# Optimization experiments

Hardware: AMD Instinct MI355X
Metric: run time of the kernel (lower is better)

The kernel has to match this reference:

```python
import jax, jax.numpy as jnp
import numpy as np

B, L, D, H = 16, 1024, 768, 12
PHD = D // H  # per-head dim = 64


def setup_inputs() -> dict:
    key = jax.random.key(0)
    ks = jax.random.split(key, 6)
    s = 0.02  # small init scale (xavier-like magnitude)
    return {
        "embeddings": jax.random.normal(ks[0], (B, L, D), jnp.float32),
        "pre_w": jax.random.normal(ks[1], (D, D), jnp.float32) * s,
        "pre_b": jnp.zeros((D,), jnp.float32),
        "psfs": jax.random.normal(ks[2], (H, 2 * L - 1, PHD), jnp.float32) * s,
        "post_w": jax.random.normal(ks[3], (D, D), jnp.float32) * s,
        "post_b": jnp.zeros((D,), jnp.float32),
        "sparse_mat": jax.random.normal(ks[4], (L, L), jnp.float32) * s,
        "ln_g": jnp.ones((D,), jnp.float32),
        "ln_b": jnp.zeros((D,), jnp.float32),
    }


def _spectral_norm(W, n_iters=1, eps=1e-12):
    # torch spectral_norm: power iteration with detached u, v; sigma = u^T W v
    u = jnp.ones((W.shape[0],), W.dtype) / jnp.sqrt(jnp.asarray(W.shape[0], W.dtype))
    for _ in range(n_iters):
        v = W.T @ u
        v = v / (jnp.linalg.norm(v) + eps)
        u = W @ v
        u = u / (jnp.linalg.norm(u) + eps)
    u = jax.lax.stop_gradient(u)
    v = jax.lax.stop_gradient(v)
    sigma = u @ (W @ v)
    return W / sigma


def reference(embeddings, pre_w, pre_b, psfs, post_w, post_b, sparse_mat, ln_g, ln_b):
    # pre-projection
    x = embeddings @ pre_w.T + pre_b                       # (B, L, D)
    # zero-pad along seq to 2L-1 and split heads
    xp = jnp.pad(x, ((0, 0), (0, L - 1), (0, 0)))          # (B, 2L-1, D)
    xp = xp.reshape(B, 2 * L - 1, H, PHD).transpose(0, 2, 1, 3)  # (B, H, 2L-1, d)
    # causal PSF mask: keep first L taps, zero the rest (zeros still enter softmax, as in torch)
    causal = (jnp.arange(2 * L - 1) < L)[None, :, None]
    psf = jnp.where(causal, psfs, 0.0)                     # (H, 2L-1, d)
    psf = jax.nn.softmax(psf, axis=1)
    # 2D circular convolution via FFT over (seq, head_dim)
    conv = jnp.fft.ifftn(jnp.fft.fftn(psf, axes=(1, 2))[None] * jnp.fft.fftn(xp, axes=(2, 3)), axes=(2, 3))
    conv = jnp.real(conv)[:, :, :L, :]                     # (B, H, L, d)
    conv = jax.nn.gelu(conv, approximate=False).transpose(0, 2, 1, 3).reshape(B, L, D)
    conv_emb = conv @ post_w.T + post_b
    # sparse branch: spectrally-normalized, causal-masked dense mixing matrix
    sp = jnp.tril(_spectral_norm(sparse_mat))              # (L, L)
    sparse_emb = jnp.einsum('st,btd->bsd', sp, x)
    # dropout is identity (eval), keep_prob = 1.0; residual + LayerNorm(eps=1e-12)
    y = conv_emb + sparse_emb + embeddings
    mu = jnp.mean(y, axis=-1, keepdims=True)
    var = jnp.mean((y - mu) ** 2, axis=-1, keepdims=True)
    return (y - mu) * jax.lax.rsqrt(var + 1e-12) * ln_g + ln_b
```

## Files before the change

kernel.cpp:

```cpp
#include <hip/hip_runtime.h>
#include <math.h>

#define Bn 16
#define Ln 1024
#define Dn 768
#define Hn 12
#define PHDn 64
#define NK 33
#define NHK (Hn * NK)
#define TWOPI_64 0.09817477042468103f

typedef short s16x8 __attribute__((ext_vector_type(8)));
typedef float f32x4 __attribute__((ext_vector_type(4)));
typedef unsigned short u16x4 __attribute__((ext_vector_type(4)));

__device__ __forceinline__ unsigned short f2bf(float f) {
    unsigned int u = __float_as_uint(f);
    unsigned int r = (u + 0x7FFFu + ((u >> 16) & 1u)) >> 16;
    return (unsigned short)r;
}
__device__ __forceinline__ float bf2f(unsigned short s) {
    unsigned int u = ((unsigned int)s) << 16;
    return __uint_as_float(u);
}
__device__ __forceinline__ float2 cmul(float2 a, float2 b) {
    return make_float2(a.x * b.x - a.y * b.y, a.x * b.y + a.y * b.x);
}
__device__ __forceinline__ float2 cadd(float2 a, float2 b) { return make_float2(a.x + b.x, a.y + b.y); }
__device__ __forceinline__ float2 csub(float2 a, float2 b) { return make_float2(a.x - b.x, a.y - b.y); }
__device__ __forceinline__ unsigned int packbf(float re, float im) {
    return (unsigned int)f2bf(re) | ((unsigned int)f2bf(im) << 16);
}
__device__ __forceinline__ float2 unpackbf(unsigned int v) {
    return make_float2(bf2f((unsigned short)(v & 0xffff)), bf2f((unsigned short)(v >> 16)));
}

#define SW(j) ((j) ^ (((j) >> 2) & 12) ^ (((j) >> 6) & 3))
#define PD(j) ((j) + ((j) >> 4))

static const size_t O_P    = 0;
static const size_t O_PSFH = 786432;
static const size_t O_PART = 1376256;
static const size_t O_QH   = 1597440;
static const size_t O_X    = 1598240;
static const size_t O_XT   = 7897888;
static const size_t O_XH   = 14189344;
static const size_t O_YH   = 27157280;
static const size_t O_SPE  = 40146080;
static const size_t O_V    = 52728992;
static const size_t O_UR   = 52730016;
static const size_t O_SIG  = 52731040;

__global__ __launch_bounds__(256) void k_psf_softmax(const float* __restrict__ psfs,
                                                     float* __restrict__ p,
                                                     float* __restrict__ q) {
    int he = blockIdx.x;
    int h = he >> 6, e = he & 63;
    int tid = threadIdx.x;
    float ev[4];
    float s = 0.f;
#pragma unroll
    for (int i = 0; i < 4; ++i) {
        int t = tid + 256 * i;
        float v = psfs[((size_t)h * 2047 + t) * 64 + e];
        ev[i] = expf(v);
        s += ev[i];
    }
    __shared__ float red[256];
    red[tid] = s; __syncthreads();
    for (int st = 128; st > 0; st >>= 1) {
        if (tid < st) red[tid] += red[tid + st];
        __syncthreads();
    }
    float denom = red[0] + 1023.0f;
    float inv = 1.0f / denom;
#pragma unroll
    for (int i = 0; i < 4; ++i) {
        int t = tid + 256 * i;
        p[((size_t)h * 1024 + t) * 64 + e] = ev[i] * inv;
    }
    if (tid == 0) q[he] = inv;
}

__global__ __launch_bounds__(256) void k_psf_dft(const float* __restrict__ p,
                                                 float* __restrict__ psfh) {
    int blk = blockIdx.x;
    int h = blk >> 8, tb = blk & 255;
    int t0 = tb * 4;
    int tid = threadIdx.x;
    int w = tid >> 6, lane = tid & 63;
    __shared__ float pv[4][64], cc[64], ssn[64];
    if (tid < 64) {
        float ang = TWOPI_64 * tid;
        cc[tid] = cosf(ang); ssn[tid] = sinf(ang);
    }
    pv[w][lane] = p[((size_t)h * 1024 + t0 + w) * 64 + lane];
    __syncthreads();
    if (lane < NK) {
        float re = 0.f, im = 0.f;
#pragma unroll 8
        for (int e = 0; e < 64; ++e) {
            int j = (lane * e) & 63;
            float v = pv[w][e];
            re += v * cc[j];
            im -= v * ssn[j];
        }
        size_t o = (((size_t)h * NK + lane) * 1024 + t0 + w) * 2;
        psfh[o] = re; psfh[o + 1] = im;
    }
}

__global__ __launch_bounds__(64) void k_q_dft(const float* __restrict__ q,
                                              float* __restrict__ qh) {
    int h = blockIdx.x;
    int tid = threadIdx.x;
    __shared__ float qv[64], cc[64], ssn[64];
    qv[tid] = q[h * 64 + tid];
    float ang = TWOPI_64 * tid;
    cc[tid] = cosf(ang); ssn[tid] = sinf(ang);
    __syncthreads();
    if (tid < NK) {
        float re = 0.f, im = 0.f;
        for (int e = 0; e < 64; ++e) {
            int j = (tid * e) & 63;
            re += qv[e] * cc[j];
            im -= qv[e] * ssn[j];
        }
        qh[(h * NK + tid) * 2] = re;
        qh[(h * NK + tid) * 2 + 1] = im;
    }
}

__device__ __forceinline__ void build_tw512(float2* tw, int tid) {
#pragma unroll
    for (int it = 0; it < 2; ++it) {
        int j = tid + it * 256;
        float a = (float)j * 3.0679615757712823e-3f;
        float sv, cv;
        __sincosf(a, &sv, &cv);
        tw[j] = make_float2(cv, -sv);
    }
}

__device__ __forceinline__ void build_tw1024(float2* tw, int tid) {
#pragma unroll
    for (int it = 0; it < 4; ++it) {
        int j = tid + it * 256;
        float a = (float)j * 3.0679615757712823e-3f;
        float sv, cv;
        __sincosf(a, &sv, &cv);
        tw[j] = make_float2(cv, -sv);
    }
}

__device__ __forceinline__ void fft_pair(const float2* __restrict__ X,
                                         float2* __restrict__ Y,
                                         const float2* __restrict__ tw,
                                         int tid, int m) {
#pragma unroll
    for (int it = 0; it < 2; ++it) {
        int i = tid + it * 256;
        int r = i & (m - 1);
        int am = i - r;
        float2 w1 = tw[am];
        float2 w1b = make_float2(w1.y, -w1.x);
        float2 w2 = cmul(w1, w1);
        float2 x0 = X[SW(i)], x1 = X[SW(i + 512)], x2 = X[SW(i + 1024)], x3 = X[SW(i + 1536)];
        float2 y0 = cadd(x0, x2);
        float2 y1 = cmul(csub(x0, x2), w1);
        float2 y2 = cadd(x1, x3);
        float2 y3 = cmul(csub(x1, x3), w1b);
        int o = 4 * am + r;
        Y[SW(o)] = cadd(y0, y2);
        Y[SW(o + m)] = cadd(y1, y3);
        Y[SW(o + 2 * m)] = cmul(csub(y0, y2), w2);
        Y[SW(o + 3 * m)] = cmul(csub(y1, y3), w2);
    }
}

__global__ __launch_bounds__(256) void k_tap_fft(const float* __restrict__ psfh,
                                                 const float* __restrict__ qh,
                                                 float* __restrict__ phf) {
    __shared__ float2 A[2048], B[2048], tw[512];
    int hk = blockIdx.x, tid = threadIdx.x;
    build_tw512(tw, tid);
    float2 qv = make_float2(qh[hk * 2], qh[hk * 2 + 1]);
    const float2* Pg = (const float2*)(psfh + (size_t)hk * 2048);
    __syncthreads();
#pragma unroll
    for (int it = 0; it < 2; ++it) {
        int i = tid + it * 256;
        float2 x0 = Pg[i], x1 = Pg[i + 512];
        float2 x2 = (i == 0) ? make_float2(0.f, 0.f) : qv;
        float2 x3 = qv;
        float2 w1 = tw[i];
        float2 w1b = make_float2(w1.y, -w1.x);
        float2 w2 = cmul(w1, w1);
        float2 y0 = cadd(x0, x2);
        float2 y1 = cmul(csub(x0, x2), w1);
        float2 y2 = cadd(x1, x3);
        float2 y3 = cmul(csub(x1, x3), w1b);
        int o = 4 * i;
        A[SW(o)] = cadd(y0, y2);
        A[SW(o + 1)] = cadd(y1, y3);
        A[SW(o + 2)] = cmul(csub(y0, y2), w2);
        A[SW(o + 3)] = cmul(csub(y1, y3), w2);
    }
    __syncthreads();
    fft_pair(A, B, tw, tid, 4);   __syncthreads();
    fft_pair(B, A, tw, tid, 16);  __syncthreads();
    fft_pair(A, B, tw, tid, 64);  __syncthreads();
    fft_pair(B, A, tw, tid, 256); __syncthreads();
    float2* out = (float2*)(phf + (size_t)hk * 4096);
#pragma unroll
    for (int it = 0; it < 4; ++it) {
        int t = tid + it * 256;
        float2 lo = A[SW(t)], hi = A[SW(t + 1024)];
        out[t] = cadd(lo, hi);
        out[t + 1024] = csub(lo, hi);
    }
}

__device__ __forceinline__ void triple_tail(float2 z0, float2 z1, float2 z2, float2 z3,
                                            float2 zz0, float2 zz1, float2 zz2, float2 zz3,
                                            float2 w2, float2 w4, float2* o) {
    float2 w2b = make_float2(w2.y, -w2.x);
    float2 a0 = cadd(z0, z2),   a2 = cmul(csub(z0, z2), w2);
    float2 b0 = cadd(z1, z3),   b2 = cmul(csub(z1, z3), w2b);
    float2 a1 = cadd(zz0, zz2), a3 = cmul(csub(zz0, zz2), w2);
    float2 b1 = cadd(zz1, zz3), b3 = cmul(csub(zz1, zz3), w2b);
    o[0] = cadd(a0, b0); o[4] = cmul(csub(a0, b0), w4);
    o[1] = cadd(a1, b1); o[5] = cmul(csub(a1, b1), w4);
    o[2] = cadd(a2, b2); o[6] = cmul(csub(a2, b2), w4);
    o[3] = cadd(a3, b3); o[7] = cmul(csub(a3, b3), w4);
}

__device__ __forceinline__ void fft_triple_lut(const float2* x, const float2* __restrict__ tw,
                                               int am, float2* o) {
    float2 w10 = tw[am], w11 = tw[am + 256];
    float2 w2 = tw[2 * am], w4 = tw[4 * am];
    float2 w10b = make_float2(w10.y, -w10.x), w11b = make_float2(w11.y, -w11.x);
    float2 z0 = cadd(x[0], x[4]), z1 = cadd(x[1], x[5]);
    float2 z2 = cadd(x[2], x[6]), z3 = cadd(x[3], x[7]);
    float2 zz0 = cmul(csub(x[0], x[4]), w10);
    float2 zz1 = cmul(csub(x[1], x[5]), w11);
    float2 zz2 = cmul(csub(x[2], x[6]), w10b);
    float2 zz3 = cmul(csub(x[3], x[7]), w11b);
    triple_tail(z0, z1, z2, z3, zz0, zz1, zz2, zz3, w2, w4, o);
}

__global__ __launch_bounds__(256) void k_conv_fft(const unsigned int* __restrict__ XHb,
                                                  const float* __restrict__ PHF,
                                                  unsigned int* __restrict__ YHb) {
    __shared__ float2 S[2176], tw[1024];
    int bhk = blockIdx.x, tid = threadIdx.x;
    int hk = bhk % NHK;
    build_tw1024(tw, tid);
    const unsigned int* Xg = XHb + (size_t)bhk * 1024;
    float2 x[8], o[8];
#pragma unroll
    for (int k = 0; k < 4; ++k) x[k] = unpackbf(Xg[tid + 256 * k]);
    __syncthreads();
    {
        float2 w10 = tw[tid], w11 = tw[tid + 256];
        float2 w2 = tw[2 * tid], w4 = tw[4 * tid];
        float2 w10b = make_float2(w10.y, -w10.x), w11b = make_float2(w11.y, -w11.x);
        float2 zz0 = cmul(x[0], w10), zz1 = cmul(x[1], w11);
        float2 zz2 = cmul(x[2], w10b), zz3 = cmul(x[3], w11b);
        triple_tail(x[0], x[1], x[2], x[3], zz0, zz1, zz2, zz3, w2, w4, o);
    }
#pragma unroll
    for (int k = 0; k < 8; ++k) S[PD(8 * tid + k)] = o[k];
    __syncthreads();
    {
        int r = tid & 7, am = tid - r;
#pragma unroll
        for (int k = 0; k < 8; ++k) x[k] = S[PD(tid + 256 * k)];
        __syncthreads();
        fft_triple_lut(x, tw, am, o);
        int base = 8 * am + r;
#pragma unroll
        for (int k = 0; k < 8; ++k) S[PD(base + 8 * k)] = o[k];
    }
    __syncthreads();
    {
        int r = tid & 63, am = tid - r;
#pragma unroll
        for (int k = 0; k < 8; ++k) x[k] = S[PD(tid + 256 * k)];
        __syncthreads();
        fft_triple_lut(x, tw, am, o);
        int base = 8 * am + r;
#pragma unroll
        for (int k = 0; k < 8; ++k) S[PD(base + 64 * k)] = o[k];
    }
    __syncthreads();
    const float2* P = (const float2*)(PHF + (size_t)hk * 4096);
    float2 v[8];
#pragma unroll
    for (int it = 0; it < 2; ++it) {
        int i2 = tid + 256 * it;
        float2 g0 = S[PD(i2)], g1 = S[PD(i2 + 512)], g2 = S[PD(i2 + 1024)], g3 = S[PD(i2 + 1536)];
        float2 y0 = cadd(g0, g2), y1 = csub(g0, g2);
        float2 y2 = cadd(g1, g3);
        float2 d13 = csub(g1, g3);
        float2 y3 = make_float2(d13.y, -d13.x);
        float2 F0 = cadd(y0, y2);
        float2 F1 = cadd(y1, y3);
        float2 F2 = csub(y0, y2);
        float2 F3 = csub(y1, y3);
        float2 V0 = cmul(F0, P[i2]);
        float2 V1 = cmul(F1, P[i2 + 512]);
        float2 V2 = cmul(F2, P[i2 + 1024]);
        float2 V3 = cmul(F3, P[i2 + 1536]);
        v[it]     = make_float2(V0.x, -V0.y);
        v[it + 2] = make_float2(V1.x, -V1.y);
        v[it + 4] = make_float2(V2.x, -V2.y);
        v[it + 6] = make_float2(V3.x, -V3.y);
    }
    __syncthreads();
    fft_triple_lut(v, tw, tid, o);
#pragma unroll
    for (int k = 0; k < 8; ++k) S[PD(8 * tid + k)] = o[k];
    __syncthreads();
    {
        int r = tid & 7, am = tid - r;
#pragma unroll
        for (int k = 0; k < 8; ++k) x[k] = S[PD(tid + 256 * k)];
        __syncthreads();
        fft_triple_lut(x, tw, am, o);
        int base = 8 * am + r;
#pragma unroll
        for (int k = 0; k < 8; ++k) S[PD(base + 8 * k)] = o[k];
    }
    __syncthreads();
    {
        int r = tid & 63, am = tid - r;
#pragma unroll
        for (int k = 0; k < 8; ++k) x[k] = S[PD(tid + 256 * k)];
        __syncthreads();
        fft_triple_lut(x, tw, am, o);
        int base = 8 * am + r;
#pragma unroll
        for (int k = 0; k < 8; ++k) S[PD(base + 64 * k)] = o[k];
    }
    __syncthreads();
    unsigned int* Yg = YHb + (size_t)bhk * 1024;
    const float inv_n = 1.0f / 2048.0f;
#pragma unroll
    for (int it = 0; it < 2; ++it) {
        int i2 = tid + 256 * it;
        float2 g0 = S[PD(i2)], g1 = S[PD(i2 + 512)], g2 = S[PD(i2 + 1024)], g3 = S[PD(i2 + 1536)];
        float2 s02 = cadd(g0, g2), d02 = csub(g0, g2);
        float2 s13 = cadd(g1, g3);
        float2 d13 = csub(g1, g3);
        float2 mj13 = make_float2(d13.y, -d13.x);
        float2 o0 = cadd(s02, s13);
        float2 o1 = cadd(d02, mj13);
        Yg[i2] = packbf(o0.x * inv_n, -o0.y * inv_n);
        Yg[i2 + 512] = packbf(o1.x * inv_n, -o1.y * inv_n);
    }
}

__global__ __launch_bounds__(64) void k_build_w(unsigned short* __restrict__ Wf,
                                                unsigned short* __restrict__ Wi) {
    int m = blockIdx.x;
    int c = threadIdx.x;
    if (m < 128) {
        float val = 0.f;
        if (m < 66) {
            int k = m >> 1, od = m & 1;
            int j = (k * c) & 63;
            float ang = TWOPI_64 * (float)j;
            val = od ? -sinf(ang) : cosf(ang);
        }
        Wf[m * 64 + c] = f2bf(val);
    } else {
        int mm = m - 128;
        float val = 0.f;
        if (mm < 64) {
            int d = mm;
            int k, od;
            float ck;
            if (c == 0)      { k = 0;  od = 0; ck = 1.f / 64.f; }
            else if (c == 1) { k = 32; od = 0; ck = 1.f / 64.f; }
            else             { k = c >> 1; od = c & 1; ck = 2.f / 64.f; }
            int j = (k * d) & 63;
            float ang = TWOPI_64 * (float)j;
            val = od ? -sinf(ang) * ck : cosf(ang) * ck;
        }
        Wi[mm * 64 + c] = f2bf(val);
    }
}

__device__ __forceinline__ void mfma_core64(const unsigned short* __restrict__ gA0,
                                            const unsigned short* __restrict__ gB0,
                                            int nkt,
                                            unsigned short* __restrict__ As,
                                            unsigned short* __restrict__ Bs,
                                            int tid, int lane, int wr, int wc,
                                            f32x4 acc[4][4]) {
    int r0 = tid >> 1, hs = (tid & 1) << 2;
    int wbase = r0 * 64;
    int swr = r0 & 7;
    int kg = lane >> 4, cl = lane & 15;
    int fra[8], frb[8];
#pragma unroll
    for (int kk = 0; kk < 2; ++kk)
#pragma unroll
        for (int i = 0; i < 4; ++i) {
            int ra = wr * 64 + i * 16 + cl;
            fra[kk * 4 + i] = ra * 64 + (((kk * 4 + kg) ^ (ra & 7)) << 3);
            int rb = wc * 64 + i * 16 + cl;
            frb[kk * 4 + i] = rb * 64 + (((kk * 4 + kg) ^ (rb & 7)) << 3);
        }
    s16x8 a[4], b[4];
#pragma unroll
    for (int l = 0; l < 4; ++l) {
        a[l] = *(const s16x8*)(gA0 + l * 8);
        b[l] = *(const s16x8*)(gB0 + l * 8);
    }
    for (int kt = 0; kt < nkt; ++kt) {
        __syncthreads();
#pragma unroll
        for (int l = 0; l < 4; ++l) {
            *(s16x8*)&As[wbase + (((hs + l) ^ swr) << 3)] = a[l];
            *(s16x8*)&Bs[wbase + (((hs + l) ^ swr) << 3)] = b[l];
        }
        __syncthreads();
        if (kt + 1 < nkt) {
            size_t ko = (size_t)(kt + 1) * 64;
#pragma unroll
            for (int l = 0; l < 4; ++l) {
                a[l] = *(const s16x8*)(gA0 + ko + l * 8);
                b[l] = *(const s16x8*)(gB0 + ko + l * 8);
            }
        }
#pragma unroll
        for (int kk = 0; kk < 2; ++kk) {
            s16x8 af[4], bfr[4];
#pragma unroll
            for (int i = 0; i < 4; ++i) af[i] = *(const s16x8*)&As[fra[kk * 4 + i]];
#pragma unroll
            for (int i = 0; i < 4; ++i) bfr[i] = *(const s16x8*)&Bs[frb[kk * 4 + i]];
#pragma unroll
            for (int mi = 0; mi < 4; ++mi)
#pragma unroll
                for (int ni = 0; ni < 4; ++ni)
                    acc[mi][ni] = __builtin_amdgcn_mfma_f32_16x16x32_bf16(af[mi], bfr[ni], acc[mi][ni], 0, 0, 0);
        }
    }
}

__global__ __launch_bounds__(512) void k_mfma_proj(const unsigned short* __restrict__ A,
                                                   const unsigned short* __restrict__ W,
                                                   const float* __restrict__ bias,
                                                   unsigned short* __restrict__ C,
                                                   unsigned short* __restrict__ XT) {
    const int K = Dn, N = Dn;
    int n0 = blockIdx.x * 256, m0 = blockIdx.y * 128;
    int tid = threadIdx.x;
    int lane = tid & 63, wave = tid >> 6;
    int wr = wave >> 2, wc = wave & 3;
    __shared__ __align__(16) unsigned short As[8192], Bs[16384];
    f32x4 acc[4][4] = {};
    int ra0 = tid >> 2, sa0 = (tid & 3) * 2;
    int rb0 = tid >> 1, sb0 = (tid & 1) * 4;
    const unsigned short* gA = A + (size_t)(m0 + ra0) * K + sa0 * 8;
    const unsigned short* gB = W + (size_t)(n0 + rb0) * K + sb0 * 8;
    int kg = lane >> 4, cl = lane & 15;
    int fra[8], frb[8];
#pragma unroll
    for (int kk = 0; kk < 2; ++kk)
#pragma unroll
        for (int i = 0; i < 4; ++i) {
            int ra = wr * 64 + i * 16 + cl;
            fra[kk * 4 + i] = ra * 64 + (((kk * 4 + kg) ^ (ra & 7)) << 3);
            int rb = wc * 64 + i * 16 + cl;
            frb[kk * 4 + i] = rb * 64 + (((kk * 4 + kg) ^ (rb & 7)) << 3);
        }
    s16x8 a[2], b[4];
#pragma unroll
    for (int l = 0; l < 2; ++l) a[l] = *(const s16x8*)(gA + l * 8);
#pragma unroll
    for (int l = 0; l < 4; ++l) b[l] = *(const s16x8*)(gB + l * 8);
    const int nkt = K >> 6;
    for (int kt = 0; kt < nkt; ++kt) {
        __syncthreads();
#pragma unroll
        for (int l = 0; l < 2; ++l)
            *(s16x8*)&As[ra0 * 64 + (((sa0 + l) ^ (ra0 & 7)) << 3)] = a[l];
#pragma unroll
        for (int l = 0; l < 4; ++l)
            *(s16x8*)&Bs[rb0 * 64 + (((sb0 + l) ^ (rb0 & 7)) << 3)] = b[l];
        __syncthreads();
        if (kt + 1 < nkt) {
            size_t ko = (size_t)(kt + 1) * 64;
#pragma unroll
            for (int l = 0; l < 2; ++l) a[l] = *(const s16x8*)(gA + ko + l * 8);
#pragma unroll
            for (int l = 0; l < 4; ++l) b[l] = *(const s16x8*)(gB + ko + l * 8);
        }
#pragma unroll
        for (int kk = 0; kk < 2; ++kk) {
            s16x8 af[4], bfr[4];
#pragma unroll
            for (int i = 0; i < 4; ++i) af[i] = *(const s16x8*)&As[fra[kk * 4 + i]];
#pragma unroll
            for (int i = 0; i < 4; ++i) bfr[i] = *(const s16x8*)&Bs[frb[kk * 4 + i]];
#pragma unroll
            for (int mi = 0; mi < 4; ++mi)
#pragma unroll
                for (int ni = 0; ni < 4; ++ni)
                    acc[mi][ni] = __builtin_amdgcn_mfma_f32_16x16x32_bf16(af[mi], bfr[ni], acc[mi][ni], 0, 0, 0);
        }
    }
    int b0 = m0 >> 10;
#pragma unroll
    for (int ni = 0; ni < 4; ++ni) {
        int gn = n0 + wc * 64 + ni * 16 + cl;
        float bv = bias[gn];
#pragma unroll
        for (int mi = 0; mi < 4; ++mi) {
            int gm = m0 + wr * 64 + mi * 16 + kg * 4;
            f32x4 v = acc[mi][ni];
            u16x4 o;
#pragma unroll
            for (int ri = 0; ri < 4; ++ri) {
                unsigned short bfv = f2bf(v[ri] + bv);
                o[ri] = bfv;
                C[(size_t)(gm + ri) * N + gn] = bfv;
            }
            if (XT) {
                int t = gm & 1023;
                *(u16x4*)&XT[((size_t)b0 * Dn + gn) * Ln + t] = o;
            }
        }
    }
}

__global__ __launch_bounds__(256) void k_mfma_dft_h(const unsigned short* __restrict__ Wf1,
                                                    const unsigned short* __restrict__ Xb,
                                                    unsigned int* __restrict__ XHb) {
    int n0 = blockIdx.x * 128;
    int h = blockIdx.y;
    int tid = threadIdx.x;
    int lane = tid & 63, wave = tid >> 6;
    int wr = wave >> 1, wc = wave & 1;
    __shared__ __align__(16) unsigned short As[8192], Bs[8192];
    f32x4 acc[4][4] = {};
    int r0 = tid >> 1, hs = (tid & 1) << 2;
    const unsigned short* gA0 = Wf1 + r0 * 64 + hs * 8;
    const unsigned short* gB0 = Xb + (size_t)(n0 + r0) * Dn + h * 64 + hs * 8;
    mfma_core64(gA0, gB0, 1, As, Bs, tid, lane, wr, wc, acc);
    int kg = lane >> 4, cl = lane & 15;
#pragma unroll
    for (int ni = 0; ni < 4; ++ni) {
        int gn = n0 + wc * 64 + ni * 16 + cl;
        int b = gn >> 10, u = gn & 1023;
#pragma unroll
        for (int mi = 0; mi < 4; ++mi) {
            int gmb = wr * 64 + mi * 16 + kg * 4;
            f32x4 v = acc[mi][ni];
#pragma unroll
            for (int rp = 0; rp < 2; ++rp) {
                int m = gmb + rp * 2;
                if (m < 66) {
                    size_t plane = (size_t)(b * Hn + h) * NK + (m >> 1);
                    XHb[plane * 1024 + u] = packbf(v[rp * 2], v[rp * 2 + 1]);
                }
            }
        }
    }
}

__global__ __launch_bounds__(256) void k_mfma_idft_h(const unsigned int* __restrict__ YHb,
                                                     const unsigned short* __restrict__ Wi1,
                                                     unsigned short* __restrict__ G) {
    int m0 = blockIdx.x * 128;
    int h = blockIdx.y;
    int b = m0 >> 10, u0 = m0 & 1023;
    int tid = threadIdx.x;
    int lane = tid & 63, wave = tid >> 6;
    int wr = wave >> 1, wc = wave & 1;
    __shared__ __align__(16) unsigned short As[8192], Bs[8192];
    int planeBase = (b * Hn + h) * NK;
#pragma unroll
    for (int i = 0; i < 17; ++i) {
        int idx = tid + i * 256;
        if (idx < 4224) {
            int k = idx >> 7, uo = idx & 127;
            unsigned int v = YHb[(size_t)(planeBase + k) * 1024 + u0 + uo];
            unsigned short lo = (unsigned short)(v & 0xffff);
            unsigned short hi = (unsigned short)(v >> 16);
            int sw = uo & 7;
            int rb = uo * 64;
            if (k == 0) {
                As[rb + (sw << 3) + 0] = lo;
            } else if (k == 32) {
                As[rb + (sw << 3) + 1] = lo;
            } else {
                int c0 = 2 * k, c1 = 2 * k + 1;
                As[rb + (((c0 >> 3) ^ sw) << 3) + (c0 & 7)] = lo;
                As[rb + (((c1 >> 3) ^ sw) << 3) + (c1 & 7)] = hi;
            }
        }
    }
    {
        int r0 = tid >> 1, hs = (tid & 1) << 2;
        int swr = r0 & 7;
        const unsigned short* gB0 = Wi1 + r0 * 64 + hs * 8;
#pragma unroll
        for (int l = 0; l < 4; ++l)
            *(s16x8*)&Bs[r0 * 64 + (((hs + l) ^ swr) << 3)] = *(const s16x8*)(gB0 + l * 8);
    }
    __syncthreads();
    f32x4 acc[4][4] = {};
    int kg = lane >> 4, cl = lane & 15;
#pragma unroll
    for (int kk = 0; kk < 2; ++kk) {
        s16x8 af[4], bfr[4];
#pragma unroll
        for (int i = 0; i < 4; ++i) {
            int ra = wr * 64 + i * 16 + cl;
            af[i] = *(const s16x8*)&As[ra * 64 + (((kk * 4 + kg) ^ (ra & 7)) << 3)];
            int rbw = wc * 64 + i * 16 + cl;
            bfr[i] = *(const s16x8*)&Bs[rbw * 64 + (((kk * 4 + kg) ^ (rbw & 7)) << 3)];
        }
#pragma unroll
        for (int mi = 0; mi < 4; ++mi)
#pragma unroll
            for (int ni = 0; ni < 4; ++ni)
                acc[mi][ni] = __builtin_amdgcn_mfma_f32_16x16x32_bf16(af[mi], bfr[ni], acc[mi][ni], 0, 0, 0);
    }
#pragma unroll
    for (int ni = 0; ni < 4; ++ni) {
        int gn = wc * 64 + ni * 16 + cl;
        if (gn < 64) {
#pragma unroll
            for (int mi = 0; mi < 4; ++mi) {
                int gm = m0 + wr * 64 + mi * 16 + kg * 4;
                f32x4 v = acc[mi][ni];
#pragma unroll
                for (int ri = 0; ri < 4; ++ri) {
                    float c = v[ri];
                    float g = c * 0.5f * (1.0f + erff(c * 0.70710678118f));
                    G[(size_t)(gm + ri) * Dn + h * 64 + gn] = f2bf(g);
                }
            }
        }
    }
}

__global__ __launch_bounds__(512) void k_mfma_sparse(const unsigned short* __restrict__ SP,
                                                     const unsigned short* __restrict__ XT,
                                                     const float* __restrict__ sigbuf,
                                                     unsigned short* __restrict__ C) {
    int bx = blockIdx.x;
    int mt = bx & 7, nt = (bx >> 3) % 3, b = bx / 24;
    int m0 = mt * 128, n0 = nt * 256;
    const unsigned short* Xb = XT + (size_t)b * Dn * Ln;
    unsigned short* Cb = C + (size_t)b * Ln * Dn;
    int tid = threadIdx.x;
    int lane = tid & 63, wave = tid >> 6;
    int wr = wave >> 2, wc = wave & 3;
    __shared__ __align__(16) unsigned short As[8192], Bs[16384];
    f32x4 acc[4][4] = {};
    int ra0 = tid >> 2, sa0 = (tid & 3) * 2;
    int rb0 = tid >> 1, sb0 = (tid & 1) * 4;
    const unsigned short* gA = SP + (size_t)(m0 + ra0) * Ln + sa0 * 8;
    const unsigned short* gB = Xb + (size_t)(n0 + rb0) * Ln + sb0 * 8;
    int kg = lane >> 4, cl = lane & 15;
    int fra[8], frb[8];
#pragma unroll
    for (int kk = 0; kk < 2; ++kk)
#pragma unroll
        for (int i = 0; i < 4; ++i) {
            int ra = wr * 64 + i * 16 + cl;
            fra[kk * 4 + i] = ra * 64 + (((kk * 4 + kg) ^ (ra & 7)) << 3);
            int rb = wc * 64 + i * 16 + cl;
            frb[kk * 4 + i] = rb * 64 + (((kk * 4 + kg) ^ (rb & 7)) << 3);
        }
    s16x8 a[2], b2[4];
#pragma unroll
    for (int l = 0; l < 2; ++l) a[l] = *(const s16x8*)(gA + l * 8);
#pragma unroll
    for (int l = 0; l < 4; ++l) b2[l] = *(const s16x8*)(gB + l * 8);
    int nkt = 2 * mt + 2;
    for (int kt = 0; kt < nkt; ++kt) {
        __syncthreads();
#pragma unroll
        for (int l = 0; l < 2; ++l)
            *(s16x8*)&As[ra0 * 64 + (((sa0 + l) ^ (ra0 & 7)) << 3)] = a[l];
#pragma unroll
        for (int l = 0; l < 4; ++l)
            *(s16x8*)&Bs[rb0 * 64 + (((sb0 + l) ^ (rb0 & 7)) << 3)] = b2[l];
        __syncthreads();
        if (kt + 1 < nkt) {
            size_t ko = (size_t)(kt + 1) * 64;
#pragma unroll
            for (int l = 0; l < 2; ++l) a[l] = *(const s16x8*)(gA + ko + l * 8);
#pragma unroll
            for (int l = 0; l < 4; ++l) b2[l] = *(const s16x8*)(gB + ko + l * 8);
        }
#pragma unroll
        for (int kk = 0; kk < 2; ++kk) {
            s16x8 af[4], bfr[4];
#pragma unroll
            for (int i = 0; i < 4; ++i) af[i] = *(const s16x8*)&As[fra[kk * 4 + i]];
#pragma unroll
            for (int i = 0; i < 4; ++i) bfr[i] = *(const s16x8*)&Bs[frb[kk * 4 + i]];
#pragma unroll
            for (int mi = 0; mi < 4; ++mi)
#pragma unroll
                for (int ni = 0; ni < 4; ++ni)
                    acc[mi][ni] = __builtin_amdgcn_mfma_f32_16x16x32_bf16(af[mi], bfr[ni], acc[mi][ni], 0, 0, 0);
        }
    }
    float invs = sigbuf[0];
#pragma unroll
    for (int ni = 0; ni < 4; ++ni) {
        int gn = n0 + wc * 64 + ni * 16 + cl;
#pragma unroll
        for (int mi = 0; mi < 4; ++mi) {
            int gm = m0 + wr * 64 + mi * 16 + kg * 4;
            f32x4 v = acc[mi][ni];
#pragma unroll
            for (int ri = 0; ri < 4; ++ri)
                Cb[(size_t)(gm + ri) * Dn + gn] = f2bf(v[ri] * invs);
        }
    }
}

__global__ __launch_bounds__(256) void k_cvt_bf16(const float* __restrict__ in,
                                                  unsigned short* __restrict__ out, int n4) {
    int i = blockIdx.x * 256 + threadIdx.x;
    if (i < n4) {
        float4 v = ((const float4*)in)[i];
        u16x4 o;
        o[0] = f2bf(v.x); o[1] = f2bf(v.y); o[2] = f2bf(v.z); o[3] = f2bf(v.w);
        *(u16x4*)&out[(size_t)i * 4] = o;
    }
}

__global__ __launch_bounds__(256) void k_sn_prep(const float* __restrict__ Wm,
                                                 float* __restrict__ partial,
                                                 unsigned short* __restrict__ SPb) {
    int b = blockIdx.x;
    int tid = threadIdx.x;
    int c0 = tid * 4;
    float4 s = make_float4(0.f, 0.f, 0.f, 0.f);
#pragma unroll
    for (int i = 0; i < 16; ++i) {
        int row = b * 16 + i;
        float4 v = *(const float4*)&Wm[(size_t)row * 1024 + c0];
        s.x += v.x; s.y += v.y; s.z += v.z; s.w += v.w;
        u16x4 o;
        o[0] = (c0 + 0 <= row) ? f2bf(v.x) : 0;
        o[1] = (c0 + 1 <= row) ? f2bf(v.y) : 0;
        o[2] = (c0 + 2 <= row) ? f2bf(v.z) : 0;
        o[3] = (c0 + 3 <= row) ? f2bf(v.w) : 0;
        *(u16x4*)&SPb[(size_t)row * 1024 + c0] = o;
    }
    *(float4*)&partial[(size_t)b * 1024 + c0] = s;
}

__global__ __launch_bounds__(1024) void k_sn_v2(const float* __restrict__ partial,
                                                float* __restrict__ v) {
    int j = threadIdx.x;
    float s = 0.f;
#pragma unroll 8
    for (int i = 0; i < 64; ++i) s += partial[(size_t)i * 1024 + j];
    s *= 0.03125f;
    __shared__ float red[1024];
    red[j] = s * s; __syncthreads();
    for (int st = 512; st > 0; st >>= 1) {
        if (j < st) red[j] += red[j + st];
        __syncthreads();
    }
    float nrm = sqrtf(red[0]);
    v[j] = s / (nrm + 1e-12f);
}

__global__ __launch_bounds__(64) void k_sn_u(const float* __restrict__ Wm,
                                             const float* __restrict__ v,
                                             float* __restrict__ ur) {
    int i = blockIdx.x;
    int lane = threadIdx.x;
    float s = 0.f;
    for (int j = lane; j < 1024; j += 64) s += Wm[(size_t)i * 1024 + j] * v[j];
#pragma unroll
    for (int off = 32; off > 0; off >>= 1) s += __shfl_down(s, off);
    if (lane == 0) ur[i] = s;
}

__global__ __launch_bounds__(1024) void k_sn_sigma(const float* __restrict__ ur,
                                                   float* __restrict__ sig) {
    int i = threadIdx.x;
    __shared__ float red[1024];
    float u = ur[i];
    red[i] = u * u; __syncthreads();
    for (int st = 512; st > 0; st >>= 1) {
        if (i < st) red[i] += red[i + st];
        __syncthreads();
    }
    if (i == 0) {
        float ss = red[0];
        float sigma = ss / (sqrtf(ss) + 1e-12f);
        sig[0] = 1.0f / sigma;
    }
}

__global__ __launch_bounds__(256) void k_final_ln(const unsigned short* __restrict__ CE,
                                                  const unsigned short* __restrict__ SE,
                                                  const unsigned short* __restrict__ EMB,
                                                  const float* __restrict__ g,
                                                  const float* __restrict__ be,
                                                  float* __restrict__ out) {
    int r = blockIdx.x;
    int tid = threadIdx.x;
    float y[3];
    float s = 0.f;
#pragma unroll
    for (int i = 0; i < 3; ++i) {
        int o = tid + i * 256;
        size_t idx = (size_t)r * 768 + o;
        y[i] = bf2f(CE[idx]) + bf2f(SE[idx]) + bf2f(EMB[idx]);
        s += y[i];
    }
    __shared__ float red[256];
    red[tid] = s; __syncthreads();
    for (int st = 128; st > 0; st >>= 1) {
        if (tid < st) red[tid] += red[tid + st];
        __syncthreads();
    }
    float mu = red[0] * (1.f / 768.f);
    __syncthreads();
    float vs = 0.f;
#pragma unroll
    for (int i = 0; i < 3; ++i) { float d = y[i] - mu; vs += d * d; }
    red[tid] = vs; __syncthreads();
    for (int st = 128; st > 0; st >>= 1) {
        if (tid < st) red[tid] += red[tid + st];
        __syncthreads();
    }
    float var = red[0] * (1.f / 768.f);
    float rstd = rsqrtf(var + 1e-12f);
#pragma unroll
    for (int i = 0; i < 3; ++i) {
        int o = tid + i * 256;
        size_t idx = (size_t)r * 768 + o;
        out[idx] = (y[i] - mu) * rstd * g[o] + be[o];
    }
}

extern "C" void kernel_launch(void* const* d_in, const int* in_sizes, int n_in,
                              void* d_out, int out_size, void* d_ws, size_t ws_size,
                              hipStream_t stream) {
    const float* emb     = (const float*)d_in[0];
    const float* pre_w   = (const float*)d_in[1];
    const float* pre_b   = (const float*)d_in[2];
    const float* psfs    = (const float*)d_in[3];
    const float* post_w  = (const float*)d_in[4];
    const float* post_b  = (const float*)d_in[5];
    const float* spmat   = (const float*)d_in[6];
    const float* ln_g    = (const float*)d_in[7];
    const float* ln_b    = (const float*)d_in[8];
    float* out = (float*)d_out;
    float* ws = (float*)d_ws;

    float* p      = ws + O_P;
    float* psfh   = ws + O_PSFH;
    float* part   = ws + O_PART;
    float* qh     = ws + O_QH;
    float* q      = ws + O_SIG + 8;
    float* phf    = ws + O_SPE;
    float* v      = ws + O_V;
    float* urw    = ws + O_UR;
    float* sig    = ws + O_SIG;

    unsigned int* XHb = (unsigned int*)(ws + O_XH);
    unsigned int* YHb = (unsigned int*)(ws + O_YH + 6291456);
    unsigned short* emb_bf    = (unsigned short*)(ws + O_YH);
    unsigned short* x_bf      = (unsigned short*)(ws + O_X);
    unsigned short* Wf1       = (unsigned short*)(ws + O_X + 6291456);
    unsigned short* Wi1       = (unsigned short*)(ws + O_X + 6295552);
    unsigned short* xT_bf     = (unsigned short*)(ws + O_XT);
    unsigned short* CE_bf     = (unsigned short*)(ws + O_XH + 6488064);
    unsigned short* spe_bf    = (unsigned short*)(ws + O_SPE);
    unsigned short* G_bf      = (unsigned short*)(ws + O_SPE + 3145728);
    unsigned short* SP_bf     = (unsigned short*)(ws + O_P);
    unsigned short* pre_w_bf  = (unsigned short*)(ws + O_PSFH);
    unsigned short* post_w_bf = (unsigned short*)(ws + O_PSFH + 294912);

    k_psf_softmax<<<Hn * 64, 256, 0, stream>>>(psfs, p, q);
    k_psf_dft<<<Hn * 256, 256, 0, stream>>>(p, psfh);
    k_q_dft<<<Hn, 64, 0, stream>>>(q, qh);
    k_tap_fft<<<NHK, 256, 0, stream>>>(psfh, qh, phf);

    k_sn_prep<<<64, 256, 0, stream>>>(spmat, part, SP_bf);
    k_sn_v2<<<1, 1024, 0, stream>>>(part, v);
    k_sn_u<<<1024, 64, 0, stream>>>(spmat, v, urw);
    k_sn_sigma<<<1, 1024, 0, stream>>>(urw, sig);

    k_cvt_bf16<<<576, 256, 0, stream>>>(pre_w, pre_w_bf, 147456);
    k_cvt_bf16<<<576, 256, 0, stream>>>(post_w, post_w_bf, 147456);
    k_cvt_bf16<<<12288, 256, 0, stream>>>(emb, emb_bf, 3145728);
    k_build_w<<<256, 64, 0, stream>>>(Wf1, Wi1);

    k_mfma_proj<<<dim3(3, 128), 512, 0, stream>>>(emb_bf, pre_w_bf, pre_b, x_bf, xT_bf);

    k_mfma_dft_h<<<dim3(128, Hn), 256, 0, stream>>>(Wf1, x_bf, XHb);

    k_conv_fft<<<Bn * NHK, 256, 0, stream>>>(XHb, phf, YHb);

    k_mfma_idft_h<<<dim3(128, Hn), 256, 0, stream>>>(YHb, Wi1, G_bf);

    k_mfma_proj<<<dim3(3, 128), 512, 0, stream>>>(G_bf, post_w_bf, post_b, CE_bf, nullptr);

    k_mfma_sparse<<<384, 512, 0, stream>>>(SP_bf, xT_bf, sig, spe_bf);

    k_final_ln<<<Bn * Ln, 256, 0, stream>>>(CE_bf, spe_bf, emb_bf, ln_g, ln_b, out);
}
```

Measured before the change: 298.3 us.

## Halve projection GEMM M-tile and stage epilogue through LDS for coalesced stores

The projection GEMM's M tile drops from 128 to 64 rows, doubling the grid from 384 to 768 blocks so more blocks run across the CUs. The epilogue now writes bias-added bf16 results into a per-wave padded LDS tile, then emits 16-byte row stores for C and 16-byte transposed stores for XT. This replaces scattered 2-byte column writes and 8-byte strided transposed writes. The cost is less B-tile reuse per block, since W is reloaded twice as often, plus extra LDS traffic and barriers in the epilogue.

```diff
diff --git a/kernel.cpp b/kernel.cpp
--- a/kernel.cpp
+++ b/kernel.cpp
@@ -457,84 +457,100 @@
                                                    unsigned short* __restrict__ C,
                                                    unsigned short* __restrict__ XT) {
     const int K = Dn, N = Dn;
-    int n0 = blockIdx.x * 256, m0 = blockIdx.y * 128;
+    int n0 = blockIdx.x * 256, m0 = blockIdx.y * 64;
     int tid = threadIdx.x;
     int lane = tid & 63, wave = tid >> 6;
     int wr = wave >> 2, wc = wave & 3;
-    __shared__ __align__(16) unsigned short As[8192], Bs[16384];
-    f32x4 acc[4][4] = {};
-    int ra0 = tid >> 2, sa0 = (tid & 3) * 2;
+    __shared__ __align__(16) unsigned short LDSu[20480];
+    unsigned short* As = LDSu;
+    unsigned short* Bs = LDSu + 4096;
+    f32x4 acc[2][4] = {};
+    int ra0 = tid >> 3, sa0 = tid & 7;
     int rb0 = tid >> 1, sb0 = (tid & 1) * 4;
     const unsigned short* gA = A + (size_t)(m0 + ra0) * K + sa0 * 8;
     const unsigned short* gB = W + (size_t)(n0 + rb0) * K + sb0 * 8;
     int kg = lane >> 4, cl = lane & 15;
-    int fra[8], frb[8];
-#pragma unroll
-    for (int kk = 0; kk < 2; ++kk)
+    int fra[4], frb[8];
+#pragma unroll
+    for (int kk = 0; kk < 2; ++kk) {
+#pragma unroll
+        for (int i = 0; i < 2; ++i) {
+            int ra = wr * 32 + i * 16 + cl;
+            fra[kk * 2 + i] = ra * 64 + (((kk * 4 + kg) ^ (ra & 7)) << 3);
+        }
 #pragma unroll
         for (int i = 0; i < 4; ++i) {
-            int ra = wr * 64 + i * 16 + cl;
-            fra[kk * 4 + i] = ra * 64 + (((kk * 4 + kg) ^ (ra & 7)) << 3);
             int rb = wc * 64 + i * 16 + cl;
             frb[kk * 4 + i] = rb * 64 + (((kk * 4 + kg) ^ (rb & 7)) << 3);
         }
-    s16x8 a[2], b[4];
-#pragma unroll
-    for (int l = 0; l < 2; ++l) a[l] = *(const s16x8*)(gA + l * 8);
+    }
+    s16x8 a0, b[4];
+    a0 = *(const s16x8*)(gA);
 #pragma unroll
     for (int l = 0; l < 4; ++l) b[l] = *(const s16x8*)(gB + l * 8);
     const int nkt = K >> 6;
     for (int kt = 0; kt < nkt; ++kt) {
         __syncthreads();
-#pragma unroll
-        for (int l = 0; l < 2; ++l)
-            *(s16x8*)&As[ra0 * 64 + (((sa0 + l) ^ (ra0 & 7)) << 3)] = a[l];
+        *(s16x8*)&As[ra0 * 64 + ((sa0 ^ (ra0 & 7)) << 3)] = a0;
 #pragma unroll
         for (int l = 0; l < 4; ++l)
             *(s16x8*)&Bs[rb0 * 64 + (((sb0 + l) ^ (rb0 & 7)) << 3)] = b[l];
         __syncthreads();
         if (kt + 1 < nkt) {
             size_t ko = (size_t)(kt + 1) * 64;
-#pragma unroll
-            for (int l = 0; l < 2; ++l) a[l] = *(const s16x8*)(gA + ko + l * 8);
+            a0 = *(const s16x8*)(gA + ko);
 #pragma unroll
             for (int l = 0; l < 4; ++l) b[l] = *(const s16x8*)(gB + ko + l * 8);
         }
 #pragma unroll
         for (int kk = 0; kk < 2; ++kk) {
-            s16x8 af[4], bfr[4];
-#pragma unroll
-            for (int i = 0; i < 4; ++i) af[i] = *(const s16x8*)&As[fra[kk * 4 + i]];
+            s16x8 af[2], bfr[4];
+#pragma unroll
+            for (int i = 0; i < 2; ++i) af[i] = *(const s16x8*)&As[fra[kk * 2 + i]];
 #pragma unroll
             for (int i = 0; i < 4; ++i) bfr[i] = *(const s16x8*)&Bs[frb[kk * 4 + i]];
 #pragma unroll
-            for (int mi = 0; mi < 4; ++mi)
+            for (int mi = 0; mi < 2; ++mi)
 #pragma unroll
                 for (int ni = 0; ni < 4; ++ni)
                     acc[mi][ni] = __builtin_amdgcn_mfma_f32_16x16x32_bf16(af[mi], bfr[ni], acc[mi][ni], 0, 0, 0);
         }
     }
-    int b0 = m0 >> 10;
+    __syncthreads();
+    unsigned short* ST = LDSu + wave * 2304;
 #pragma unroll
     for (int ni = 0; ni < 4; ++ni) {
         int gn = n0 + wc * 64 + ni * 16 + cl;
         float bv = bias[gn];
 #pragma unroll
-        for (int mi = 0; mi < 4; ++mi) {
-            int gm = m0 + wr * 64 + mi * 16 + kg * 4;
+        for (int mi = 0; mi < 2; ++mi) {
             f32x4 v = acc[mi][ni];
-            u16x4 o;
-#pragma unroll
-            for (int ri = 0; ri < 4; ++ri) {
-                unsigned short bfv = f2bf(v[ri] + bv);
-                o[ri] = bfv;
-                C[(size_t)(gm + ri) * N + gn] = bfv;
-            }
-            if (XT) {
-                int t = gm & 1023;
-                *(u16x4*)&XT[((size_t)b0 * Dn + gn) * Ln + t] = o;
-            }
-        }
+#pragma unroll
+            for (int ri = 0; ri < 4; ++ri)
+                ST[(mi * 16 + kg * 4 + ri) * 72 + ni * 16 + cl] = f2bf(v[ri] + bv);
+        }
+    }
+    __syncthreads();
+    {
+        int r = lane >> 1, ch = (lane & 1) * 32;
+        int gm = m0 + wr * 32 + r;
+        const unsigned short* src = ST + r * 72 + ch;
+        unsigned short* dst = C + (size_t)gm * N + n0 + wc * 64 + ch;
+#pragma unroll
+        for (int j = 0; j < 4; ++j)
+            *(s16x8*)(dst + j * 8) = *(const s16x8*)(src + j * 8);
+    }
+    if (XT) {
+        int gn = n0 + wc * 64 + lane;
+        unsigned short tmp[32];
+#pragma unroll
+        for (int r = 0; r < 32; ++r) tmp[r] = ST[r * 72 + lane];
+        int b0 = m0 >> 10;
+        int t0 = (m0 & 1023) + wr * 32;
+        unsigned short* dst = XT + ((size_t)b0 * Dn + gn) * Ln + t0;
+#pragma unroll
+        for (int j = 0; j < 4; ++j)
+            *(s16x8*)(dst + j * 8) = *(const s16x8*)&tmp[j * 8];
     }
 }
 
@@ -907,7 +923,7 @@
     k_cvt_bf16<<<12288, 256, 0, stream>>>(emb, emb_bf, 3145728);
     k_build_w<<<256, 64, 0, stream>>>(Wf1, Wi1);
 
-    k_mfma_proj<<<dim3(3, 128), 512, 0, stream>>>(emb_bf, pre_w_bf, pre_b, x_bf, xT_bf);
+    k_mfma_proj<<<dim3(3, 256), 512, 0, stream>>>(emb_bf, pre_w_bf, pre_b, x_bf, xT_bf);
 
     k_mfma_dft_h<<<dim3(128, Hn), 256, 0, stream>>>(Wf1, x_bf, XHb);
 
@@ -915,7 +931,7 @@
 
     k_mfma_idft_h<<<dim3(128, Hn), 256, 0, stream>>>(YHb, Wi1, G_bf);
 
-    k_mfma_proj<<<dim3(3, 128), 512, 0, stream>>>(G_bf, post_w_bf, post_b, CE_bf, nullptr);
+    k_mfma_proj<<<dim3(3, 256), 512, 0, stream>>>(G_bf, post_w_bf, post_b, CE_bf, nullptr);
 
     k_mfma_sparse<<<384, 512, 0, stream>>>(SP_bf, xT_bf, sig, spe_bf);
 
```

After: 294.5 us, median of 2. No clear change (-1.3%).
